# Kernel optimization log

Measured on AMD Instinct MI355X. Metric: run time of the kernel, lower is better.

The kernel has to match this reference:

```python
import jax, jax.numpy as jnp
import numpy as np

S = 32        # num_subdomains
D = 1         # in_size
WIDTH = 128   # width_size
DEPTH = 4     # eqx MLP depth -> 1 input layer + (DEPTH-1) hidden layers + 1 output layer
N = 262144    # collocation points
TOL = 1e-8


def setup_inputs() -> dict:
    key = jax.random.key(0)
    ks = jax.random.split(key, 7)
    # subdomain i = [(i-0.5)/S, (i+1.5)/S] -> center (i+0.5)/S, half-width 1/S
    centers = ((jnp.arange(S, dtype=jnp.float32) + 0.5) / S)[:, None]          # (S, D)
    scales = jnp.full((S, D), 1.0 / S, dtype=jnp.float32)                       # (S, D)

    def unif(k, shape, fan_in):  # equinox Linear init: U(-1/sqrt(fan_in), 1/sqrt(fan_in))
        lim = 1.0 / np.sqrt(fan_in)
        return jax.random.uniform(k, shape, jnp.float32, -lim, lim)

    W_in = unif(ks[0], (S, WIDTH, D), D)
    b_in = unif(ks[1], (S, WIDTH), D)
    W_hid = unif(ks[2], (S, DEPTH - 1, WIDTH, WIDTH), WIDTH)
    b_hid = unif(ks[3], (S, DEPTH - 1, WIDTH), WIDTH)
    W_out = unif(ks[4], (S, 1, WIDTH), WIDTH)
    b_out = unif(ks[5], (S, 1), WIDTH)
    x = jax.random.uniform(ks[6], (N, D), jnp.float32, 0.0, 1.0)
    return {"x": x, "W_in": W_in, "b_in": b_in, "W_hid": W_hid, "b_hid": b_hid,
            "W_out": W_out, "b_out": b_out, "centers": centers, "scales": scales}


def reference(x, W_in, b_in, W_hid, b_hid, W_out, b_out, centers, scales):
    # normalized coords per subdomain: (S, n, D)
    u = (x[None, :, :] - centers[:, None, :]) / scales[:, None, :]
    # partition-of-unity cosine window, product over dims, normalized over subdomains
    raw = jnp.prod(jnp.where(jnp.abs(u) < 1.0, jnp.cos(0.5 * jnp.pi * u) ** 2, 0.0), axis=-1)  # (S, n)
    w = raw / (jnp.sum(raw, axis=0, keepdims=True) + TOL)                                       # (S, n)

    def body(total, p):
        Wi, bi, Wh, bh, Wo, bo, xn, wk = p
        h = jnp.tanh(xn @ Wi.T + bi)                      # (n, WIDTH)
        for l in range(DEPTH - 1):                        # static unroll over hidden layers
            h = jnp.tanh(h @ Wh[l].T + bh[l])
        out = (h @ Wo.T + bo)[:, 0]                       # (n,)
        return total + wk * out, None

    total, _ = jax.lax.scan(body, jnp.zeros(x.shape[0], x.dtype),
                            (W_in, b_in, W_hid, b_hid, W_out, b_out, u, w))
    # ansatz = identity
    return total
```

## Files before the change

kernel.cpp:

```cpp
#include <hip/hip_runtime.h>

#define NS 32
#define WID 128
#define NHID 3
#define NPTS 262144
#define PTILE 256
#define TMLP 512
#define CAP 17408
#define TPB (CAP / PTILE)

#define TASKS_OFF 512
#define WF_OFF (TASKS_OFF + NS * CAP * 4)
#define TANH_C 2.8853900817779268f

typedef _Float16 f16x2 __attribute__((ext_vector_type(2)));
typedef _Float16 f16x4 __attribute__((ext_vector_type(4)));
typedef _Float16 f16x8 __attribute__((ext_vector_type(8)));
typedef __fp16 fp16x2 __attribute__((ext_vector_type(2)));
typedef float f32x4 __attribute__((ext_vector_type(4)));

union U4H8 { uint4 u; f16x8 h; };
union PK2 { fp16x2 p; f16x2 h; };

__device__ __forceinline__ f16x2 pk2(float a, float b) {
    PK2 u; u.p = __builtin_amdgcn_cvt_pkrtz(a, b); return u.h;
}

__device__ __forceinline__ float tanh_fast(float v) {
    float a = v * TANH_C;
    float e; asm("v_exp_f32 %0, %1" : "=v"(e) : "v"(a));
    float d = e + 1.0f;
    float r; asm("v_rcp_f32 %0, %1" : "=v"(r) : "v"(d));
    return fmaf(-2.0f, r, 1.0f);
}

__device__ __forceinline__ float tanh_pre(float a) {
    float e; asm("v_exp_f32 %0, %1" : "=v"(e) : "v"(a));
    float d = e + 1.0f;
    float r; asm("v_rcp_f32 %0, %1" : "=v"(r) : "v"(d));
    return fmaf(-2.0f, r, 1.0f);
}

__device__ __forceinline__ float coswin(float u) {
    if (fabsf(u) >= 1.0f) return 0.0f;
    float rev = u * 0.25f;
    float c; asm("v_cos_f32 %0, %1" : "=v"(c) : "v"(rev));
    return c * c;
}


__global__ void k_scatter2(const float* __restrict__ x, int* __restrict__ cursors,
                           int* __restrict__ tasks, float* __restrict__ out, int n) {
    __shared__ int loc[NS];
    __shared__ int base[NS];
    int t = threadIdx.x;
    if (t < NS) loc[t] = 0;
    __syncthreads();
    int i = blockIdx.x * blockDim.x + t;
    int j = -1, nb = -1, sj = 0, snb = 0;
    if (i < n) {
        out[i] = 0.0f;
        float tt = x[i] * 32.0f;
        j = min(max((int)floorf(tt), 0), 31);
        sj = atomicAdd(&loc[j], 1);
        float u = tt - (float)j - 0.5f;
        int nb2 = (u > 0.0f) ? j + 1 : j - 1;
        if (u != 0.0f && nb2 >= 0 && nb2 < NS) { nb = nb2; snb = atomicAdd(&loc[nb], 1); }
    }
    __syncthreads();
    if (t < NS) base[t] = atomicAdd(&cursors[t], loc[t]);
    __syncthreads();
    if (i < n) {
        tasks[j * CAP + base[j] + sj] = i;
        if (nb >= 0) tasks[nb * CAP + base[nb] + snb] = i;
    }
}


__global__ void k_prepw(const float* __restrict__ Wh, uint4* __restrict__ WfU4) {
    int tid = blockIdx.x * blockDim.x + threadIdx.x;
    if (tid >= 32 * 3 * 8 * 4 * 64) return;
    int lane = tid & 63;
    int s    = (tid >> 6) & 3;
    int t8   = (tid >> 8) & 7;
    int v    = tid >> 11;
    int o    = 16 * t8 + (lane & 15);
    const float* src = Wh + ((size_t)v * 128 + o) * 128;
    unsigned short b[8];
#pragma unroll
    for (int e = 0; e < 8; ++e) {
        int k = 32 * s + 4 * (lane >> 4) + (e & 3) + 16 * (e >> 2);
        _Float16 hv = (_Float16)(src[k] * TANH_C);
        b[e] = *(unsigned short*)&hv;
    }
    uint4 outv;
    outv.x = (unsigned)b[0] | ((unsigned)b[1] << 16);
    outv.y = (unsigned)b[2] | ((unsigned)b[3] << 16);
    outv.z = (unsigned)b[4] | ((unsigned)b[5] << 16);
    outv.w = (unsigned)b[6] | ((unsigned)b[7] << 16);
    WfU4[((size_t)(v * 8 + t8) * 4 + s) * 64 + lane] = outv;
}


__global__ __launch_bounds__(TMLP, 4) void k_mlp(
    const float* __restrict__ x, const float* __restrict__ W_in, const float* __restrict__ b_in,
    const float* __restrict__ b_hid, const float* __restrict__ W_out, const float* __restrict__ b_out,
    const float* __restrict__ centers, const float* __restrict__ scales,
    const int* __restrict__ cursors, const int* __restrict__ tasks,
    const uint4* __restrict__ WfU4, float* __restrict__ out) {

    const int bin = blockIdx.y;
    const int tile = blockIdx.x;
    const int cnt = cursors[bin];
    if (tile * PTILE >= cnt) return;
    const int start = bin * CAP;

    __shared__ __align__(256) _Float16 HT[8][4096];
    __shared__ float lU[PTILE], lWgt[PTILE];
    __shared__ int lTid[PTILE];

    const int t = threadIdx.x;
    const int lane = t & 63;
    const int l15 = t & 15;
    const int g = (t >> 4) & 3;
    const int w = t >> 6;

    if (t < PTILE) {
        int idx = tile * PTILE + t;
        if (idx < cnt) {
            int pid = tasks[start + idx];
            lTid[t] = pid;
            float xx = x[pid];
            float u = (xx - centers[bin]) * (1.0f / scales[bin]);
            lU[t] = u;
            float rs = coswin(u);
            int other = bin + (u > 0.0f ? 1 : -1);
            float ro = 0.0f;
            if (other >= 0 && other < NS)
                ro = coswin((xx - centers[other]) * (1.0f / scales[other]));
            lWgt[t] = rs / (rs + ro + 1e-8f);
        } else { lTid[t] = -1; lU[t] = 0.0f; lWgt[t] = 0.0f; }
    }
    __syncthreads();

    const uint4* wfbase = WfU4 + (size_t)(bin * NHID) * 32 * 64 + lane;

    uint4 bufA[4], bufB[4];
#pragma unroll
    for (int s = 0; s < 4; ++s) bufA[s] = wfbase[s * 64];

    {
        float4 ua = *(const float4*)&lU[w * 32 + 4 * g];
        float4 ub = *(const float4*)&lU[w * 32 + 16 + 4 * g];
        const float* Win = W_in + bin * WID;
        const float* Bi  = b_in + bin * WID;
#pragma unroll
        for (int t8 = 0; t8 < 8; ++t8) {
            int o = 16 * t8 + l15;
            float wv = Win[o], bv = Bi[o];
            f16x2 h00 = pk2(tanh_fast(fmaf(ua.x, wv, bv)), tanh_fast(fmaf(ua.y, wv, bv)));
            f16x2 h01 = pk2(tanh_fast(fmaf(ua.z, wv, bv)), tanh_fast(fmaf(ua.w, wv, bv)));
            f16x2 h10 = pk2(tanh_fast(fmaf(ub.x, wv, bv)), tanh_fast(fmaf(ub.y, wv, bv)));
            f16x2 h11 = pk2(tanh_fast(fmaf(ub.z, wv, bv)), tanh_fast(fmaf(ub.w, wv, bv)));
            *(f16x4*)&HT[w][o * 16 + 4 * g] = __builtin_shufflevector(h00, h01, 0, 1, 2, 3);
            *(f16x4*)&HT[w][2048 + o * 16 + 4 * g] = __builtin_shufflevector(h10, h11, 0, 1, 2, 3);
        }
    }

    const unsigned htaddr = (unsigned)(size_t)&HT[w][0] + lane * 8;
    float p0 = 0.f, p1 = 0.f, p2 = 0.f, p3 = 0.f;
    float q0 = 0.f, q1 = 0.f, q2 = 0.f, q3 = 0.f;

#pragma unroll
    for (int lyr = 0; lyr < NHID; ++lyr) {
        const float* bh = b_hid + (size_t)(bin * NHID + lyr) * WID;
        float bhv[8], wov[8];
#pragma unroll
        for (int t8 = 0; t8 < 8; ++t8) bhv[t8] = bh[16 * t8 + l15] * TANH_C;
        if (lyr == NHID - 1) {
#pragma unroll
            for (int t8 = 0; t8 < 8; ++t8) wov[t8] = W_out[bin * WID + 16 * t8 + l15];
        }

        f16x4 r0, r1, r2, r3, r4, r5, r6, r7, r8, r9, r10, r11, r12, r13, r14, r15;
        asm volatile(
            "ds_read_b64_tr_b16 %0, %16 offset:0\n\t"
            "ds_read_b64_tr_b16 %1, %16 offset:512\n\t"
            "ds_read_b64_tr_b16 %2, %16 offset:1024\n\t"
            "ds_read_b64_tr_b16 %3, %16 offset:1536\n\t"
            "ds_read_b64_tr_b16 %4, %16 offset:2048\n\t"
            "ds_read_b64_tr_b16 %5, %16 offset:2560\n\t"
            "ds_read_b64_tr_b16 %6, %16 offset:3072\n\t"
            "ds_read_b64_tr_b16 %7, %16 offset:3584\n\t"
            "ds_read_b64_tr_b16 %8, %16 offset:4096\n\t"
            "ds_read_b64_tr_b16 %9, %16 offset:4608\n\t"
            "ds_read_b64_tr_b16 %10, %16 offset:5120\n\t"
            "ds_read_b64_tr_b16 %11, %16 offset:5632\n\t"
            "ds_read_b64_tr_b16 %12, %16 offset:6144\n\t"
            "ds_read_b64_tr_b16 %13, %16 offset:6656\n\t"
            "ds_read_b64_tr_b16 %14, %16 offset:7168\n\t"
            "ds_read_b64_tr_b16 %15, %16 offset:7680\n\t"
            "s_waitcnt lgkmcnt(0)"
            : "=v"(r0), "=v"(r1), "=v"(r2), "=v"(r3), "=v"(r4), "=v"(r5), "=v"(r6), "=v"(r7),
              "=v"(r8), "=v"(r9), "=v"(r10), "=v"(r11), "=v"(r12), "=v"(r13), "=v"(r14), "=v"(r15)
            : "v"(htaddr) : "memory");
        f16x8 A0[4], A1[4];
        A0[0] = __builtin_shufflevector(r0, r1, 0, 1, 2, 3, 4, 5, 6, 7);
        A0[1] = __builtin_shufflevector(r2, r3, 0, 1, 2, 3, 4, 5, 6, 7);
        A0[2] = __builtin_shufflevector(r4, r5, 0, 1, 2, 3, 4, 5, 6, 7);
        A0[3] = __builtin_shufflevector(r6, r7, 0, 1, 2, 3, 4, 5, 6, 7);
        A1[0] = __builtin_shufflevector(r8, r9, 0, 1, 2, 3, 4, 5, 6, 7);
        A1[1] = __builtin_shufflevector(r10, r11, 0, 1, 2, 3, 4, 5, 6, 7);
        A1[2] = __builtin_shufflevector(r12, r13, 0, 1, 2, 3, 4, 5, 6, 7);
        A1[3] = __builtin_shufflevector(r14, r15, 0, 1, 2, 3, 4, 5, 6, 7);

        const uint4* wfL = wfbase + (size_t)lyr * 32 * 64;
        const uint4* wfN = wfbase + (size_t)(lyr + 1) * 32 * 64;

#pragma unroll
        for (int tp = 0; tp < 4; ++tp) {
            const int t8a = 2 * tp, t8b = 2 * tp + 1;
#pragma unroll
            for (int s = 0; s < 4; ++s) bufB[s] = wfL[(t8b * 4 + s) * 64];

            f32x4 acc0 = (f32x4){0.f, 0.f, 0.f, 0.f};
            f32x4 acc1 = (f32x4){0.f, 0.f, 0.f, 0.f};
            __builtin_amdgcn_s_setprio(1);
#pragma unroll
            for (int s = 0; s < 4; ++s) {
                U4H8 bw; bw.u = bufA[s];
                acc0 = __builtin_amdgcn_mfma_f32_16x16x32_f16(A0[s], bw.h, acc0, 0, 0, 0);
                acc1 = __builtin_amdgcn_mfma_f32_16x16x32_f16(A1[s], bw.h, acc1, 0, 0, 0);
            }
            __builtin_amdgcn_s_setprio(0);

            if (lyr < NHID - 1) {
                int o = 16 * t8a + l15;
                float bv = bhv[t8a];
                f16x2 h00 = pk2(tanh_pre(acc0[0] + bv), tanh_pre(acc0[1] + bv));
                f16x2 h01 = pk2(tanh_pre(acc0[2] + bv), tanh_pre(acc0[3] + bv));
                f16x2 h10 = pk2(tanh_pre(acc1[0] + bv), tanh_pre(acc1[1] + bv));
                f16x2 h11 = pk2(tanh_pre(acc1[2] + bv), tanh_pre(acc1[3] + bv));
                *(f16x4*)&HT[w][o * 16 + 4 * g] = __builtin_shufflevector(h00, h01, 0, 1, 2, 3);
                *(f16x4*)&HT[w][2048 + o * 16 + 4 * g] = __builtin_shufflevector(h10, h11, 0, 1, 2, 3);
            } else {
                float bv = bhv[t8a], wv = wov[t8a];
                p0 = fmaf(wv, tanh_pre(acc0[0] + bv), p0);
                p1 = fmaf(wv, tanh_pre(acc0[1] + bv), p1);
                p2 = fmaf(wv, tanh_pre(acc0[2] + bv), p2);
                p3 = fmaf(wv, tanh_pre(acc0[3] + bv), p3);
                q0 = fmaf(wv, tanh_pre(acc1[0] + bv), q0);
                q1 = fmaf(wv, tanh_pre(acc1[1] + bv), q1);
                q2 = fmaf(wv, tanh_pre(acc1[2] + bv), q2);
                q3 = fmaf(wv, tanh_pre(acc1[3] + bv), q3);
            }

            if (t8b < 7) {
#pragma unroll
                for (int s = 0; s < 4; ++s) bufA[s] = wfL[((t8b + 1) * 4 + s) * 64];
            } else if (lyr < NHID - 1) {
#pragma unroll
                for (int s = 0; s < 4; ++s) bufA[s] = wfN[s * 64];
            }

            f32x4 bcc0 = (f32x4){0.f, 0.f, 0.f, 0.f};
            f32x4 bcc1 = (f32x4){0.f, 0.f, 0.f, 0.f};
            __builtin_amdgcn_s_setprio(1);
#pragma unroll
            for (int s = 0; s < 4; ++s) {
                U4H8 bw; bw.u = bufB[s];
                bcc0 = __builtin_amdgcn_mfma_f32_16x16x32_f16(A0[s], bw.h, bcc0, 0, 0, 0);
                bcc1 = __builtin_amdgcn_mfma_f32_16x16x32_f16(A1[s], bw.h, bcc1, 0, 0, 0);
            }
            __builtin_amdgcn_s_setprio(0);

            if (lyr < NHID - 1) {
                int o = 16 * t8b + l15;
                float bv = bhv[t8b];
                f16x2 h00 = pk2(tanh_pre(bcc0[0] + bv), tanh_pre(bcc0[1] + bv));
                f16x2 h01 = pk2(tanh_pre(bcc0[2] + bv), tanh_pre(bcc0[3] + bv));
                f16x2 h10 = pk2(tanh_pre(bcc1[0] + bv), tanh_pre(bcc1[1] + bv));
                f16x2 h11 = pk2(tanh_pre(bcc1[2] + bv), tanh_pre(bcc1[3] + bv));
                *(f16x4*)&HT[w][o * 16 + 4 * g] = __builtin_shufflevector(h00, h01, 0, 1, 2, 3);
                *(f16x4*)&HT[w][2048 + o * 16 + 4 * g] = __builtin_shufflevector(h10, h11, 0, 1, 2, 3);
            } else {
                float bv = bhv[t8b], wv = wov[t8b];
                p0 = fmaf(wv, tanh_pre(bcc0[0] + bv), p0);
                p1 = fmaf(wv, tanh_pre(bcc0[1] + bv), p1);
                p2 = fmaf(wv, tanh_pre(bcc0[2] + bv), p2);
                p3 = fmaf(wv, tanh_pre(bcc0[3] + bv), p3);
                q0 = fmaf(wv, tanh_pre(bcc1[0] + bv), q0);
                q1 = fmaf(wv, tanh_pre(bcc1[1] + bv), q1);
                q2 = fmaf(wv, tanh_pre(bcc1[2] + bv), q2);
                q3 = fmaf(wv, tanh_pre(bcc1[3] + bv), q3);
            }
        }
    }

#pragma unroll
    for (int m = 1; m < 16; m <<= 1) {
        p0 += __shfl_xor(p0, m); p1 += __shfl_xor(p1, m);
        p2 += __shfl_xor(p2, m); p3 += __shfl_xor(p3, m);
        q0 += __shfl_xor(q0, m); q1 += __shfl_xor(q1, m);
        q2 += __shfl_xor(q2, m); q3 += __shfl_xor(q3, m);
    }
    if (l15 < 4) {
        float bo = b_out[bin];
        float v0 = ((l15 == 0) ? p0 : (l15 == 1) ? p1 : (l15 == 2) ? p2 : p3) + bo;
        float v1 = ((l15 == 0) ? q0 : (l15 == 1) ? q1 : (l15 == 2) ? q2 : q3) + bo;
        int pl0 = w * 32 + 4 * g + l15;
        int pl1 = pl0 + 16;
        int pid0 = lTid[pl0], pid1 = lTid[pl1];
        if (pid0 >= 0) atomicAdd(out + pid0, lWgt[pl0] * v0);
        if (pid1 >= 0) atomicAdd(out + pid1, lWgt[pl1] * v1);
    }
}

extern "C" void kernel_launch(void* const* d_in, const int* in_sizes, int n_in,
                              void* d_out, int out_size, void* d_ws, size_t ws_size,
                              hipStream_t stream) {
    const float* x       = (const float*)d_in[0];
    const float* W_in    = (const float*)d_in[1];
    const float* b_in    = (const float*)d_in[2];
    const float* W_hid   = (const float*)d_in[3];
    const float* b_hid   = (const float*)d_in[4];
    const float* W_out   = (const float*)d_in[5];
    const float* b_out   = (const float*)d_in[6];
    const float* centers = (const float*)d_in[7];
    const float* scales  = (const float*)d_in[8];
    float* out = (float*)d_out;

    char* ws = (char*)d_ws;
    int* cursors = (int*)(ws);
    int* tasks   = (int*)(ws + TASKS_OFF);
    uint4* WfU4  = (uint4*)(ws + WF_OFF);

    (void)hipMemsetAsync(ws, 0, 256, stream);

    k_prepw<<<dim3(768), dim3(256), 0, stream>>>(W_hid, WfU4);
    k_scatter2<<<dim3(NPTS / 256), dim3(256), 0, stream>>>(x, cursors, tasks, out, NPTS);
    k_mlp<<<dim3(TPB, NS), dim3(TMLP), 0, stream>>>(x, W_in, b_in, b_hid, W_out, b_out,
                                                    centers, scales, cursors, tasks,
                                                    WfU4, out);
}
```

Measured before the change: 117.0 us.

## Fuse weight prep and scatter into one kernel; stage weight transpose via LDS

Merges the fp16 weight repacking kernel and the point-binning scatter kernel into a single launch, using block index to pick the role, so one kernel launch and its gap are removed. The weight repack now reads coalesced float4 rows into a padded LDS tile and writes the MFMA-fragment layout from LDS, instead of doing strided global reads. In the MLP kernel, hidden-bias loads move after the LDS transposed reads and output-weight values are loaded at point of use rather than held in registers, which lowers register pressure at the cost of extra global/cache loads inside the loop.

```diff
diff --git a/kernel.cpp b/kernel.cpp
--- a/kernel.cpp
+++ b/kernel.cpp
@@ -21,6 +21,7 @@
 
 union U4H8 { uint4 u; f16x8 h; };
 union PK2 { fp16x2 p; f16x2 h; };
+union H4U2 { f16x4 h; uint2 u; };
 
 __device__ __forceinline__ f16x2 pk2(float a, float b) {
     PK2 u; u.p = __builtin_amdgcn_cvt_pkrtz(a, b); return u.h;
@@ -49,56 +50,63 @@
 }
 
 
-__global__ void k_scatter2(const float* __restrict__ x, int* __restrict__ cursors,
-                           int* __restrict__ tasks, float* __restrict__ out, int n) {
+__global__ __launch_bounds__(256) void k_prep(
+    const float* __restrict__ Wh, uint4* __restrict__ WfU4,
+    const float* __restrict__ x, int* __restrict__ cursors,
+    int* __restrict__ tasks, float* __restrict__ out, int n) {
+    __shared__ _Float16 sW[128 * 132];
     __shared__ int loc[NS];
     __shared__ int base[NS];
-    int t = threadIdx.x;
-    if (t < NS) loc[t] = 0;
-    __syncthreads();
-    int i = blockIdx.x * blockDim.x + t;
-    int j = -1, nb = -1, sj = 0, snb = 0;
-    if (i < n) {
-        out[i] = 0.0f;
-        float tt = x[i] * 32.0f;
-        j = min(max((int)floorf(tt), 0), 31);
-        sj = atomicAdd(&loc[j], 1);
-        float u = tt - (float)j - 0.5f;
-        int nb2 = (u > 0.0f) ? j + 1 : j - 1;
-        if (u != 0.0f && nb2 >= 0 && nb2 < NS) { nb = nb2; snb = atomicAdd(&loc[nb], 1); }
-    }
-    __syncthreads();
-    if (t < NS) base[t] = atomicAdd(&cursors[t], loc[t]);
-    __syncthreads();
-    if (i < n) {
-        tasks[j * CAP + base[j] + sj] = i;
-        if (nb >= 0) tasks[nb * CAP + base[nb] + snb] = i;
-    }
-}
-
-
-__global__ void k_prepw(const float* __restrict__ Wh, uint4* __restrict__ WfU4) {
-    int tid = blockIdx.x * blockDim.x + threadIdx.x;
-    if (tid >= 32 * 3 * 8 * 4 * 64) return;
-    int lane = tid & 63;
-    int s    = (tid >> 6) & 3;
-    int t8   = (tid >> 8) & 7;
-    int v    = tid >> 11;
-    int o    = 16 * t8 + (lane & 15);
-    const float* src = Wh + ((size_t)v * 128 + o) * 128;
-    unsigned short b[8];
-#pragma unroll
-    for (int e = 0; e < 8; ++e) {
-        int k = 32 * s + 4 * (lane >> 4) + (e & 3) + 16 * (e >> 2);
-        _Float16 hv = (_Float16)(src[k] * TANH_C);
-        b[e] = *(unsigned short*)&hv;
-    }
-    uint4 outv;
-    outv.x = (unsigned)b[0] | ((unsigned)b[1] << 16);
-    outv.y = (unsigned)b[2] | ((unsigned)b[3] << 16);
-    outv.z = (unsigned)b[4] | ((unsigned)b[5] << 16);
-    outv.w = (unsigned)b[6] | ((unsigned)b[7] << 16);
-    WfU4[((size_t)(v * 8 + t8) * 4 + s) * 64 + lane] = outv;
+    const int b = blockIdx.x;
+    const int t = threadIdx.x;
+    if (b < 96) {
+        const float* src = Wh + (size_t)b * 16384;
+#pragma unroll
+        for (int it = 0; it < 16; ++it) {
+            int idx = it * 1024 + t * 4;
+            int o = idx >> 7, c = idx & 127;
+            float4 v = *(const float4*)(src + idx);
+            f16x4 hv;
+            hv[0] = (_Float16)(v.x * TANH_C);
+            hv[1] = (_Float16)(v.y * TANH_C);
+            hv[2] = (_Float16)(v.z * TANH_C);
+            hv[3] = (_Float16)(v.w * TANH_C);
+            *(f16x4*)&sW[o * 132 + c] = hv;
+        }
+        __syncthreads();
+#pragma unroll
+        for (int it = 0; it < 8; ++it) {
+            int f = it * 256 + t;
+            int lane = f & 63, s = (f >> 6) & 3, t8 = f >> 8;
+            int o = 16 * t8 + (lane & 15), h = lane >> 4;
+            H4U2 lo, hi;
+            lo.h = *(f16x4*)&sW[o * 132 + 32 * s + 4 * h];
+            hi.h = *(f16x4*)&sW[o * 132 + 32 * s + 4 * h + 16];
+            uint4 outv = {lo.u.x, lo.u.y, hi.u.x, hi.u.y};
+            WfU4[(size_t)b * 2048 + f] = outv;
+        }
+    } else {
+        if (t < NS) loc[t] = 0;
+        __syncthreads();
+        int i = (b - 96) * 256 + t;
+        int j = -1, nb = -1, sj = 0, snb = 0;
+        if (i < n) {
+            out[i] = 0.0f;
+            float tt = x[i] * 32.0f;
+            j = min(max((int)floorf(tt), 0), 31);
+            sj = atomicAdd(&loc[j], 1);
+            float u = tt - (float)j - 0.5f;
+            int nb2 = (u > 0.0f) ? j + 1 : j - 1;
+            if (u != 0.0f && nb2 >= 0 && nb2 < NS) { nb = nb2; snb = atomicAdd(&loc[nb], 1); }
+        }
+        __syncthreads();
+        if (t < NS) base[t] = atomicAdd(&cursors[t], loc[t]);
+        __syncthreads();
+        if (i < n) {
+            tasks[j * CAP + base[j] + sj] = i;
+            if (nb >= 0) tasks[nb * CAP + base[nb] + snb] = i;
+        }
+    }
 }
 
 
@@ -173,15 +181,6 @@
 
 #pragma unroll
     for (int lyr = 0; lyr < NHID; ++lyr) {
-        const float* bh = b_hid + (size_t)(bin * NHID + lyr) * WID;
-        float bhv[8], wov[8];
-#pragma unroll
-        for (int t8 = 0; t8 < 8; ++t8) bhv[t8] = bh[16 * t8 + l15] * TANH_C;
-        if (lyr == NHID - 1) {
-#pragma unroll
-            for (int t8 = 0; t8 < 8; ++t8) wov[t8] = W_out[bin * WID + 16 * t8 + l15];
-        }
-
         f16x4 r0, r1, r2, r3, r4, r5, r6, r7, r8, r9, r10, r11, r12, r13, r14, r15;
         asm volatile(
             "ds_read_b64_tr_b16 %0, %16 offset:0\n\t"
@@ -214,6 +213,11 @@
         A1[2] = __builtin_shufflevector(r12, r13, 0, 1, 2, 3, 4, 5, 6, 7);
         A1[3] = __builtin_shufflevector(r14, r15, 0, 1, 2, 3, 4, 5, 6, 7);
 
+        const float* bh = b_hid + (size_t)(bin * NHID + lyr) * WID;
+        float bhv[8];
+#pragma unroll
+        for (int t8 = 0; t8 < 8; ++t8) bhv[t8] = bh[16 * t8 + l15] * TANH_C;
+
         const uint4* wfL = wfbase + (size_t)lyr * 32 * 64;
         const uint4* wfN = wfbase + (size_t)(lyr + 1) * 32 * 64;
 
@@ -244,7 +248,7 @@
                 *(f16x4*)&HT[w][o * 16 + 4 * g] = __builtin_shufflevector(h00, h01, 0, 1, 2, 3);
                 *(f16x4*)&HT[w][2048 + o * 16 + 4 * g] = __builtin_shufflevector(h10, h11, 0, 1, 2, 3);
             } else {
-                float bv = bhv[t8a], wv = wov[t8a];
+                float bv = bhv[t8a], wv = W_out[bin * WID + 16 * t8a + l15];
                 p0 = fmaf(wv, tanh_pre(acc0[0] + bv), p0);
                 p1 = fmaf(wv, tanh_pre(acc0[1] + bv), p1);
                 p2 = fmaf(wv, tanh_pre(acc0[2] + bv), p2);
@@ -284,7 +288,7 @@
                 *(f16x4*)&HT[w][o * 16 + 4 * g] = __builtin_shufflevector(h00, h01, 0, 1, 2, 3);
                 *(f16x4*)&HT[w][2048 + o * 16 + 4 * g] = __builtin_shufflevector(h10, h11, 0, 1, 2, 3);
             } else {
-                float bv = bhv[t8b], wv = wov[t8b];
+                float bv = bhv[t8b], wv = W_out[bin * WID + 16 * t8b + l15];
                 p0 = fmaf(wv, tanh_pre(bcc0[0] + bv), p0);
                 p1 = fmaf(wv, tanh_pre(bcc0[1] + bv), p1);
                 p2 = fmaf(wv, tanh_pre(bcc0[2] + bv), p2);
@@ -337,8 +341,8 @@
 
     (void)hipMemsetAsync(ws, 0, 256, stream);
 
-    k_prepw<<<dim3(768), dim3(256), 0, stream>>>(W_hid, WfU4);
-    k_scatter2<<<dim3(NPTS / 256), dim3(256), 0, stream>>>(x, cursors, tasks, out, NPTS);
+    k_prep<<<dim3(96 + NPTS / 256), dim3(256), 0, stream>>>(W_hid, WfU4, x, cursors,
+                                                            tasks, out, NPTS);
     k_mlp<<<dim3(TPB, NS), dim3(TMLP), 0, stream>>>(x, W_in, b_in, b_hid, W_out, b_out,
                                                     centers, scales, cursors, tasks,
                                                     WfU4, out);
```

Result: faster. 113.3 us (-3.1%).
